# Optimization experiments

Hardware: AMD Instinct MI355X
Metric: run time of the kernel (lower is better)

The kernel has to match this reference:

```python
import jax, jax.numpy as jnp
import numpy as np

N0, N1, N2 = 200000, 100000, 50000
E0, E1 = 1600000, 800000
D_IN, H, C, K = 256, 256, 7, 40  # in_feats, n_hidden, center_num, n_classes


def setup_inputs() -> dict:
    key = jax.random.key(0)
    ks = jax.random.split(key, 11)
    s = 0.05
    inputs = jax.random.normal(ks[0], (N0, D_IN), jnp.float32)
    edge_src0 = jax.random.randint(ks[1], (E0,), 0, N0, jnp.int32)
    edge_dst0 = jax.random.randint(ks[2], (E0,), 0, N1, jnp.int32)
    edge_src1 = jax.random.randint(ks[3], (E1,), 0, N1, jnp.int32)
    edge_dst1 = jax.random.randint(ks[4], (E1,), 0, N2, jnp.int32)
    W_self0 = jax.random.normal(ks[5], (H, D_IN), jnp.float32) * s
    W_neigh0 = jax.random.normal(ks[6], (H, D_IN), jnp.float32) * s
    b0 = jnp.zeros((H,), jnp.float32)
    W_self1 = jax.random.normal(ks[7], (H, H), jnp.float32) * s
    W_neigh1 = jax.random.normal(ks[8], (H, H), jnp.float32) * s
    b1 = jnp.zeros((H,), jnp.float32)
    W_prompt = jax.random.normal(ks[9], (C, 2 * H), jnp.float32) * s
    W_pp = jax.random.normal(ks[10], (C, K, 2 * H), jnp.float32) * s
    return dict(inputs=inputs, W_self0=W_self0, W_neigh0=W_neigh0, b0=b0,
                W_self1=W_self1, W_neigh1=W_neigh1, b1=b1,
                W_prompt=W_prompt, W_pp=W_pp,
                edge_src0=edge_src0, edge_dst0=edge_dst0,
                edge_src1=edge_src1, edge_dst1=edge_dst1)


def _sage_conv(h_src, h_dst, esrc, edst, n_dst, W_self, W_neigh, b):
    # DGL SAGEConv('mean'): fc_self(h_dst) + fc_neigh(mean_{u in N(v)} h_src[u]) + bias
    msg = h_src[esrc]                                            # [E, d]
    summ = jax.ops.segment_sum(msg, edst, num_segments=n_dst)    # [n_dst, d]
    deg = jax.ops.segment_sum(jnp.ones((esrc.shape[0],), msg.dtype), edst,
                              num_segments=n_dst)                # [n_dst]
    mean = summ / jnp.maximum(deg, 1.0)[:, None]
    return h_dst @ W_self.T + mean @ W_neigh.T + b


def _forward(inputs, W_self0, W_neigh0, b0, W_self1, W_neigh1, b1,
             W_prompt, W_pp, edge_src0, edge_dst0, edge_src1, edge_dst1):
    h = inputs  # dropout=0.0 (eval): identity
    # layer 0: N0 src -> N1 dst
    h_dst = h[:N1]
    h = _sage_conv(h, h_dst, edge_src0, edge_dst0, N1, W_self0, W_neigh0, b0)
    h = jax.nn.relu(h)
    # layer 1: N1 src -> N2 dst
    h_dst = h[:N2]
    h = _sage_conv(h, h_dst, edge_src1, edge_dst1, N2, W_self1, W_neigh1, b1)
    h = jax.nn.relu(h)
    neighbor = jax.nn.relu(h_dst)
    hcat = jnp.concatenate([h, neighbor], axis=1)                # [N2, 2H]
    scores = hcat @ W_prompt.T                                   # [N2, C]
    index = jnp.argmax(scores, axis=1)                           # [N2]
    # per-cluster expert Linear, top-1 dispatch/combine
    all_out = jnp.einsum('nd,ckd->nck', hcat, W_pp)              # [N2, C, K]
    out = jnp.take_along_axis(all_out, index[:, None, None], axis=1)[:, 0, :]
    return out


def reference(inputs, W_self0, W_neigh0, b0, W_self1, W_neigh1, b1,
              W_prompt, W_pp, edge_src0, edge_dst0, edge_src1, edge_dst1):
    return _forward(inputs, W_self0, W_neigh0, b0, W_self1, W_neigh1, b1,
                    W_prompt, W_pp, edge_src0, edge_dst0, edge_src1, edge_dst1)
```

## Files before the change

kernel.cpp:

```cpp
#include <hip/hip_runtime.h>
#include <stdint.h>

typedef unsigned short u16;
typedef unsigned int   u32;
typedef float f32x4  __attribute__((ext_vector_type(4)));
typedef _Float16 f16x4 __attribute__((ext_vector_type(4)));
typedef _Float16 f16x8 __attribute__((ext_vector_type(8)));

#define NN0 200000
#define NN1 100000
#define NN2 50000
#define EE0 1600000
#define EE1 800000
#define DD  256
#define CC  7
#define KK  40
#define NHEAD 288

#define LVL2_U16 4096
#define IMG_U16  8192

static __device__ __forceinline__ void split2(float x, _Float16& t0, _Float16& t1) {
    t0 = (_Float16)x;
    t1 = (_Float16)(x - (float)t0);
}

static __device__ __forceinline__ f16x8 pack8(const _Float16* h) {
    f16x8 v;
#pragma unroll
    for (int i = 0; i < 8; ++i) v[i] = h[i];
    return v;
}

static __device__ __forceinline__ void async16(const void* g, void* l) {
    __builtin_amdgcn_global_load_lds(
        (const __attribute__((address_space(1))) void*)g,
        (__attribute__((address_space(3))) void*)l, 16, 0, 0);
}

static __device__ __forceinline__ void loadA_f32(const float* p, float* xa) {
#pragma unroll
    for (int j = 0; j < 16; j += 4) {
        float4 v = *reinterpret_cast<const float4*>(p + j);
        xa[j] = v.x; xa[j + 1] = v.y; xa[j + 2] = v.z; xa[j + 3] = v.w;
    }
}

static __device__ __forceinline__ void writeA_f32(const float* xa, u16* d, int q0, int q1) {
    _Float16 h0[16], h1v[16];
#pragma unroll
    for (int j = 0; j < 16; ++j) split2(xa[j], h0[j], h1v[j]);
    *reinterpret_cast<f16x8*>(d + q0 * 8)            = pack8(h0);
    *reinterpret_cast<f16x8*>(d + q1 * 8)            = pack8(h0 + 8);
    *reinterpret_cast<f16x8*>(d + LVL2_U16 + q0 * 8) = pack8(h1v);
    *reinterpret_cast<f16x8*>(d + LVL2_U16 + q1 * 8) = pack8(h1v + 8);
}

__global__ void hist_kernel(const int* __restrict__ dst, int* __restrict__ cnt, int n) {
    int i = blockIdx.x * blockDim.x + threadIdx.x;
    if (i < n) atomicAdd(&cnt[dst[i]], 1);
}

__global__ void scan_block_kernel(const int* __restrict__ in, int* __restrict__ out,
                                  int* __restrict__ partials, int n) {
    __shared__ int sd[256];
    int t = threadIdx.x;
    int base = blockIdx.x * 1024 + t * 4;
    int v0 = (base + 0 < n) ? in[base + 0] : 0;
    int v1 = (base + 1 < n) ? in[base + 1] : 0;
    int v2 = (base + 2 < n) ? in[base + 2] : 0;
    int v3 = (base + 3 < n) ? in[base + 3] : 0;
    int p0 = v0, p1 = p0 + v1, p2 = p1 + v2, p3 = p2 + v3;
    sd[t] = p3;
    __syncthreads();
    for (int off = 1; off < 256; off <<= 1) {
        int x = (t >= off) ? sd[t - off] : 0;
        __syncthreads();
        sd[t] += x;
        __syncthreads();
    }
    int excl = sd[t] - p3;
    if (base + 0 < n) out[base + 0] = excl + p0;
    if (base + 1 < n) out[base + 1] = excl + p1;
    if (base + 2 < n) out[base + 2] = excl + p2;
    if (base + 3 < n) out[base + 3] = excl + p3;
    if (t == 255) partials[blockIdx.x] = sd[255];
}

__global__ void scan_partials_kernel(int* __restrict__ partials, int nb) {
    __shared__ int sd[256];
    int t = threadIdx.x;
    int v = (t < nb) ? partials[t] : 0;
    sd[t] = v;
    __syncthreads();
    for (int off = 1; off < 256; off <<= 1) {
        int x = (t >= off) ? sd[t - off] : 0;
        __syncthreads();
        sd[t] += x;
        __syncthreads();
    }
    if (t < nb) partials[t] = sd[t];
}

__global__ void scan_add_kernel(int* __restrict__ out, const int* __restrict__ partials, int n) {
    int b = blockIdx.x;
    if (b == 0) return;
    int add = partials[b - 1];
    int base = b * 1024 + threadIdx.x * 4;
    if (base + 0 < n) out[base + 0] += add;
    if (base + 1 < n) out[base + 1] += add;
    if (base + 2 < n) out[base + 2] += add;
    if (base + 3 < n) out[base + 3] += add;
}

__global__ void fill_kernel(const int* __restrict__ esrc, const int* __restrict__ edst,
                            const int* __restrict__ rp, int* __restrict__ cur,
                            int* __restrict__ ss, int n) {
    int i = blockIdx.x * blockDim.x + threadIdx.x;
    if (i < n) {
        int d = edst[i];
        int p = rp[d] + atomicAdd(&cur[d], 1);
        ss[p] = esrc[i];
    }
}

__global__ void to_fp16(const float* __restrict__ in, _Float16* __restrict__ outp, long n) {
    long i = ((long)blockIdx.x * blockDim.x + threadIdx.x) * 8;
    if (i >= n) return;
    f32x4 a = *reinterpret_cast<const f32x4*>(in + i);
    f32x4 b = *reinterpret_cast<const f32x4*>(in + i + 4);
    f16x8 h;
    h[0] = (_Float16)a[0]; h[1] = (_Float16)a[1]; h[2] = (_Float16)a[2]; h[3] = (_Float16)a[3];
    h[4] = (_Float16)b[0]; h[5] = (_Float16)b[1]; h[6] = (_Float16)b[2]; h[7] = (_Float16)b[3];
    *reinterpret_cast<f16x8*>(outp + i) = h;
}

__global__ void gather_mean_fp16(const _Float16* __restrict__ Xh, const int* __restrict__ rp,
                                 const int* __restrict__ ss, float* __restrict__ mean, int ndst) {
    int wave = threadIdx.x >> 6, lane = threadIdx.x & 63;
    int d = blockIdx.x * 4 + wave;
    if (d >= ndst) return;
    int beg = rp[d], end = rp[d + 1];
    int lo4 = lane * 4;
    f32x4 a0 = (f32x4)(0.f), a1 = (f32x4)(0.f), a2 = (f32x4)(0.f), a3 = (f32x4)(0.f);
    int j = beg;
    for (; j + 8 <= end; j += 8) {
        int s0 = ss[j + 0], s1 = ss[j + 1], s2 = ss[j + 2], s3 = ss[j + 3];
        int s4 = ss[j + 4], s5 = ss[j + 5], s6 = ss[j + 6], s7 = ss[j + 7];
        f16x4 h0 = *reinterpret_cast<const f16x4*>(Xh + (size_t)s0 * DD + lo4);
        f16x4 h1 = *reinterpret_cast<const f16x4*>(Xh + (size_t)s1 * DD + lo4);
        f16x4 h2 = *reinterpret_cast<const f16x4*>(Xh + (size_t)s2 * DD + lo4);
        f16x4 h3 = *reinterpret_cast<const f16x4*>(Xh + (size_t)s3 * DD + lo4);
        f16x4 h4 = *reinterpret_cast<const f16x4*>(Xh + (size_t)s4 * DD + lo4);
        f16x4 h5 = *reinterpret_cast<const f16x4*>(Xh + (size_t)s5 * DD + lo4);
        f16x4 h6 = *reinterpret_cast<const f16x4*>(Xh + (size_t)s6 * DD + lo4);
        f16x4 h7 = *reinterpret_cast<const f16x4*>(Xh + (size_t)s7 * DD + lo4);
        a0 += __builtin_convertvector(h0, f32x4);
        a1 += __builtin_convertvector(h1, f32x4);
        a2 += __builtin_convertvector(h2, f32x4);
        a3 += __builtin_convertvector(h3, f32x4);
        a0 += __builtin_convertvector(h4, f32x4);
        a1 += __builtin_convertvector(h5, f32x4);
        a2 += __builtin_convertvector(h6, f32x4);
        a3 += __builtin_convertvector(h7, f32x4);
    }
    for (; j + 4 <= end; j += 4) {
        int s0 = ss[j + 0], s1 = ss[j + 1], s2 = ss[j + 2], s3 = ss[j + 3];
        f16x4 h0 = *reinterpret_cast<const f16x4*>(Xh + (size_t)s0 * DD + lo4);
        f16x4 h1 = *reinterpret_cast<const f16x4*>(Xh + (size_t)s1 * DD + lo4);
        f16x4 h2 = *reinterpret_cast<const f16x4*>(Xh + (size_t)s2 * DD + lo4);
        f16x4 h3 = *reinterpret_cast<const f16x4*>(Xh + (size_t)s3 * DD + lo4);
        a0 += __builtin_convertvector(h0, f32x4);
        a1 += __builtin_convertvector(h1, f32x4);
        a2 += __builtin_convertvector(h2, f32x4);
        a3 += __builtin_convertvector(h3, f32x4);
    }
    for (; j < end; ++j) {
        int s = ss[j];
        f16x4 h0 = *reinterpret_cast<const f16x4*>(Xh + (size_t)s * DD + lo4);
        a0 += __builtin_convertvector(h0, f32x4);
    }
    f32x4 s = (a0 + a1) + (a2 + a3);
    int dg = end - beg;
    float inv = 1.0f / (float)(dg > 0 ? dg : 1);
    s *= inv;
    *reinterpret_cast<f32x4*>(mean + (size_t)d * DD + lo4) = s;
}

__global__ void build_wimg(const float* __restrict__ Wa0, const float* __restrict__ Wb0,
                           const float* __restrict__ Wa1, const float* __restrict__ Wb1,
                           u16* __restrict__ img) {
    int blk = blockIdx.x;
    int layer = blk >> 5;
    int ntile = (blk >> 4) & 1;
    int chunk = blk & 15;
    const float* Wa = layer ? Wa1 : Wa0;
    const float* Wb = layer ? Wb1 : Wb0;
    int t = threadIdx.x;
    int row = t >> 1, half = t & 1;
    int n = ntile * 128 + row;
    int kg = chunk * 32 + half * 16;
    const float* W = (kg < 256) ? Wa : Wb;
    int kk = kg & 255;
    float x[16];
    loadA_f32(W + (size_t)n * 256 + kk, x);
    int rs = (row >> 1) & 3;
    int q0 = (half * 2 + 0) ^ rs;
    int q1 = (half * 2 + 1) ^ rs;
    writeA_f32(x, img + (size_t)blk * IMG_U16 + row * 32, q0, q1);
}

__global__ void build_wimg_head(const float* __restrict__ Wp, const float* __restrict__ Wpp,
                                u16* __restrict__ img) {
    int blk = blockIdx.x;
    int ntile = blk >> 4;
    int chunk = blk & 15;
    int t = threadIdx.x;
    int row = t >> 1, half = t & 1;
    int r = ntile * 128 + row;
    int kg = chunk * 32 + half * 16;
    float x[16];
    const float* src = nullptr;
    if (r < CC)                src = Wp  + (size_t)r * 512 + kg;
    else if (r < CC + CC * KK) src = Wpp + (size_t)(r - CC) * 512 + kg;
    if (src) loadA_f32(src, x);
    else {
#pragma unroll
        for (int j = 0; j < 16; ++j) x[j] = 0.f;
    }
    int rs = (row >> 1) & 3;
    int q0 = (half * 2 + 0) ^ rs;
    int q1 = (half * 2 + 1) ^ rs;
    writeA_f32(x, img + (size_t)blk * IMG_U16 + row * 32, q0, q1);
}

__global__ __launch_bounds__(256, 3) void gemm_f16(const float* __restrict__ X0,
                                                   const float* __restrict__ X1,
                                                   const u16* __restrict__ imgL,
                                                   const float* __restrict__ bias,
                                                   float* __restrict__ out,
                                                   _Float16* __restrict__ outh,
                                                   int M, int ldo, int dorelu) {
    __shared__ __align__(16) u16 Asl[2 * LVL2_U16];
    __shared__ __align__(16) u16 Bsl[2][2 * LVL2_U16];
    int t = threadIdx.x;
    int wave = t >> 6, lane = t & 63;
    int m0 = blockIdx.x * 128;
    int ntile = blockIdx.y;
    int wy = wave >> 1, wx = wave & 1;

    f32x4 acc[4][4];
#pragma unroll
    for (int i = 0; i < 4; ++i)
#pragma unroll
        for (int j = 0; j < 4; ++j) acc[i][j] = (f32x4)(0.f);

    int arow_l = t >> 1;
    int akh = t & 1;
    int arow = m0 + arow_l; if (arow >= M) arow = M - 1;
    int rsw = (arow_l >> 1) & 3;
    int q0w = (akh * 2 + 0) ^ rsw;
    int q1w = (akh * 2 + 1) ^ rsw;

    int fr = lane & 15;
    int q  = lane >> 4;
    int frm = wy * 64 + fr;
    int frn = wx * 64 + fr;

    const u16* imgT = imgL + (size_t)ntile * 16 * IMG_U16;

    float xa[16];

    auto issueB = [&](int cc, int buf) {
        const char* srcB = (const char*)(imgT + (size_t)cc * IMG_U16);
        char* dstB = (char*)Bsl[buf];
#pragma unroll
        for (int i = 0; i < 4; ++i) {
            int seg = wave * 4 + i;
            async16(srcB + seg * 1024 + lane * 16, dstB + seg * 1024 + lane * 16);
        }
    };
    auto loadA = [&](int cc) {
        const float* Xs = (cc < 8) ? X0 : X1;
        loadA_f32(Xs + (size_t)arow * 256 + (cc & 7) * 32 + akh * 16, xa);
    };
    auto writeA = [&]() {
        writeA_f32(xa, Asl + arow_l * 32, q0w, q1w);
    };

    issueB(0, 0);
    loadA(0);
    writeA();
    __syncthreads();

    for (int c = 0; c < 16; ++c) {
        int nc = c + 1;
        if (nc < 16) {
            issueB(nc, nc & 1);
            loadA(nc);
        }
        const u16* B = Bsl[c & 1];
        f16x8 bf[4][2];
#pragma unroll
        for (int ns = 0; ns < 4; ++ns) {
            int r = frn + ns * 16;
            int off = r * 32 + ((q ^ ((r >> 1) & 3))) * 8;
            bf[ns][0] = *reinterpret_cast<const f16x8*>(B + off);
            bf[ns][1] = *reinterpret_cast<const f16x8*>(B + LVL2_U16 + off);
        }
#pragma unroll
        for (int ms = 0; ms < 4; ++ms) {
            int r = frm + ms * 16;
            int off = r * 32 + ((q ^ ((r >> 1) & 3))) * 8;
            f16x8 af0 = *reinterpret_cast<const f16x8*>(Asl + off);
            f16x8 af1 = *reinterpret_cast<const f16x8*>(Asl + LVL2_U16 + off);
#pragma unroll
            for (int ns = 0; ns < 4; ++ns) {
                f32x4 a = acc[ms][ns];
                a = __builtin_amdgcn_mfma_f32_16x16x32_f16(af0, bf[ns][0], a, 0, 0, 0);
                a = __builtin_amdgcn_mfma_f32_16x16x32_f16(af0, bf[ns][1], a, 0, 0, 0);
                a = __builtin_amdgcn_mfma_f32_16x16x32_f16(af1, bf[ns][0], a, 0, 0, 0);
                acc[ms][ns] = a;
            }
        }
        __syncthreads();
        if (nc < 16) {
            writeA();
            __syncthreads();
        }
    }
#pragma unroll
    for (int ms = 0; ms < 4; ++ms) {
        int rbase = m0 + wy * 64 + ms * 16 + (lane >> 4) * 4;
#pragma unroll
        for (int ns = 0; ns < 4; ++ns) {
            int col = ntile * 128 + wx * 64 + ns * 16 + (lane & 15);
            if (col >= ldo) continue;
            float bcol = bias ? bias[col] : 0.f;
#pragma unroll
            for (int r = 0; r < 4; ++r) {
                int row = rbase + r;
                if (row < M) {
                    float v = acc[ms][ns][r] + bcol;
                    if (dorelu) v = fmaxf(v, 0.f);
                    out[(size_t)row * ldo + col] = v;
                    if (outh) outh[(size_t)row * DD + col] = (_Float16)v;
                }
            }
        }
    }
}

__global__ void select_kernel(const float* __restrict__ all, float* __restrict__ out) {
    int wave = threadIdx.x >> 6, lane = threadIdx.x & 63;
    int n = blockIdx.x * 4 + wave;
    if (n >= NN2) return;
    const float* row = all + (size_t)n * NHEAD;
    float best = row[0]; int bc = 0;
#pragma unroll
    for (int c = 1; c < CC; ++c) {
        float s = row[c];
        if (s > best) { best = s; bc = c; }
    }
    if (lane < KK) out[(size_t)n * KK + lane] = row[CC + bc * KK + lane];
}

extern "C" void kernel_launch(void* const* d_in, const int* in_sizes, int n_in,
                              void* d_out, int out_size, void* d_ws, size_t ws_size,
                              hipStream_t stream) {
    const float* inputs  = (const float*)d_in[0];
    const float* Wself0  = (const float*)d_in[1];
    const float* Wneigh0 = (const float*)d_in[2];
    const float* b0      = (const float*)d_in[3];
    const float* Wself1  = (const float*)d_in[4];
    const float* Wneigh1 = (const float*)d_in[5];
    const float* b1      = (const float*)d_in[6];
    const float* Wp      = (const float*)d_in[7];
    const float* Wpp     = (const float*)d_in[8];
    const int* es0 = (const int*)d_in[9];
    const int* ed0 = (const int*)d_in[10];
    const int* es1 = (const int*)d_in[11];
    const int* ed1 = (const int*)d_in[12];

    char* ws = (char*)d_ws;
    size_t off = 0;
    auto alloc = [&](size_t bytes) -> void* {
        void* p = (void*)(ws + off);
        off += (bytes + 255) & ~(size_t)255;
        return p;
    };
    int* cnt0 = (int*)alloc((size_t)NN1 * 4);
    int* cnt1 = (int*)alloc((size_t)NN2 * 4);
    int* cur0 = (int*)alloc((size_t)NN1 * 4);
    int* cur1 = (int*)alloc((size_t)NN2 * 4);
    int* rp0  = (int*)alloc((size_t)(NN1 + 1) * 4);
    int* rp1  = (int*)alloc((size_t)(NN2 + 1) * 4);
    int* part0 = (int*)alloc(1024);
    int* part1 = (int*)alloc(1024);
    size_t zero_bytes = off;
    int*   ss0   = (int*)alloc((size_t)EE0 * 4);
    int*   ss1   = (int*)alloc((size_t)EE1 * 4);
    u16*   wimg  = (u16*)alloc((size_t)(64 + 48) * IMG_U16 * 2);
    u16*   wimgH = wimg + (size_t)64 * IMG_U16;
    _Float16* xh = (_Float16*)alloc((size_t)NN0 * DD * 2);
    float*    h1 = (float*)xh;
    _Float16* h1h  = (_Float16*)alloc((size_t)NN1 * DD * 2);
    float* mean0 = (float*)alloc((size_t)NN1 * DD * 4);
    float* mean1 = mean0;
    float* h2    = mean0 + (size_t)NN2 * DD;
    float* allout = (float*)alloc((size_t)NN2 * NHEAD * 4);

    hipMemsetAsync(d_ws, 0, zero_bytes, stream);

    hist_kernel<<<(EE0 + 255) / 256, 256, 0, stream>>>(ed0, cnt0, EE0);
    hist_kernel<<<(EE1 + 255) / 256, 256, 0, stream>>>(ed1, cnt1, EE1);
    int nb0 = (NN1 + 1023) / 1024, nb1 = (NN2 + 1023) / 1024;
    scan_block_kernel<<<nb0, 256, 0, stream>>>(cnt0, rp0 + 1, part0, NN1);
    scan_partials_kernel<<<1, 256, 0, stream>>>(part0, nb0);
    scan_add_kernel<<<nb0, 256, 0, stream>>>(rp0 + 1, part0, NN1);
    scan_block_kernel<<<nb1, 256, 0, stream>>>(cnt1, rp1 + 1, part1, NN2);
    scan_partials_kernel<<<1, 256, 0, stream>>>(part1, nb1);
    scan_add_kernel<<<nb1, 256, 0, stream>>>(rp1 + 1, part1, NN2);
    fill_kernel<<<(EE0 + 255) / 256, 256, 0, stream>>>(es0, ed0, rp0, cur0, ss0, EE0);
    fill_kernel<<<(EE1 + 255) / 256, 256, 0, stream>>>(es1, ed1, rp1, cur1, ss1, EE1);

    build_wimg<<<64, 256, 0, stream>>>(Wself0, Wneigh0, Wself1, Wneigh1, wimg);
    build_wimg_head<<<48, 256, 0, stream>>>(Wp, Wpp, wimgH);

    long nx = (long)NN0 * DD;
    to_fp16<<<(int)(nx / 8 / 256), 256, 0, stream>>>(inputs, xh, nx);

    gather_mean_fp16<<<(NN1 + 3) / 4, 256, 0, stream>>>(xh, rp0, ss0, mean0, NN1);
    dim3 g0((NN1 + 127) / 128, 2);
    gemm_f16<<<g0, 256, 0, stream>>>(inputs, mean0, wimg, b0, h1, h1h, NN1, DD, 1);

    gather_mean_fp16<<<(NN2 + 3) / 4, 256, 0, stream>>>(h1h, rp1, ss1, mean1, NN2);
    dim3 g1((NN2 + 127) / 128, 2);
    gemm_f16<<<g1, 256, 0, stream>>>(h1, mean1, wimg + (size_t)32 * IMG_U16, b1, h2, nullptr, NN2, DD, 1);

    dim3 gh((NN2 + 127) / 128, 3);
    gemm_f16<<<gh, 256, 0, stream>>>(h2, h1, wimgH, nullptr, allout, nullptr, NN2, NHEAD, 0);
    select_kernel<<<(NN2 + 3) / 4, 256, 0, stream>>>(allout, (float*)d_out);
}
```

Measured before the change: 1.084 ms.

## Pre-split activations into swizzled fp16 hi/lo tile images for async GEMM A loads

Producers (fp16 conversion, gather-mean, and GEMM epilogues) now write activations directly as pre-swizzled hi/lo fp16 tile images, so the GEMM can load A via async global-to-LDS copies like B instead of loading fp32 and splitting in registers. The GEMM loop drops double-buffering in favour of a single buffer with a sync per chunk and raises the occupancy hint to 4 blocks. This removes per-block fp32 loads and split work from the GEMM but doubles activation storage writes and loses load/compute overlap within a block.

```diff
diff --git a/kernel.cpp b/kernel.cpp
--- a/kernel.cpp
+++ b/kernel.cpp
@@ -19,6 +19,7 @@
 
 #define LVL2_U16 4096
 #define IMG_U16  8192
+#define AIMG_STRIDE (8 * IMG_U16)
 
 static __device__ __forceinline__ void split2(float x, _Float16& t0, _Float16& t1) {
     t0 = (_Float16)x;
@@ -124,19 +125,31 @@
     }
 }
 
-__global__ void to_fp16(const float* __restrict__ in, _Float16* __restrict__ outp, long n) {
+__global__ void to_fp16_split(const float* __restrict__ in, _Float16* __restrict__ xh,
+                              u16* __restrict__ imgX, long n) {
     long i = ((long)blockIdx.x * blockDim.x + threadIdx.x) * 8;
     if (i >= n) return;
     f32x4 a = *reinterpret_cast<const f32x4*>(in + i);
     f32x4 b = *reinterpret_cast<const f32x4*>(in + i + 4);
-    f16x8 h;
-    h[0] = (_Float16)a[0]; h[1] = (_Float16)a[1]; h[2] = (_Float16)a[2]; h[3] = (_Float16)a[3];
-    h[4] = (_Float16)b[0]; h[5] = (_Float16)b[1]; h[6] = (_Float16)b[2]; h[7] = (_Float16)b[3];
-    *reinterpret_cast<f16x8*>(outp + i) = h;
+    float x[8] = {a[0], a[1], a[2], a[3], b[0], b[1], b[2], b[3]};
+    _Float16 t0[8], t1[8];
+#pragma unroll
+    for (int j = 0; j < 8; ++j) split2(x[j], t0[j], t1[j]);
+    *reinterpret_cast<f16x8*>(xh + i) = pack8(t0);
+    int row = (int)(i >> 8);
+    if (row < NN1) {
+        int k = (int)(i & 255);
+        int lrow = row & 127, ch = k >> 5;
+        int qs = ((k & 31) >> 3) ^ ((lrow >> 1) & 3);
+        u16* p = imgX + (size_t)(row >> 7) * AIMG_STRIDE + (size_t)ch * IMG_U16
+               + lrow * 32 + qs * 8;
+        *reinterpret_cast<f16x8*>(p)            = pack8(t0);
+        *reinterpret_cast<f16x8*>(p + LVL2_U16) = pack8(t1);
+    }
 }
 
 __global__ void gather_mean_fp16(const _Float16* __restrict__ Xh, const int* __restrict__ rp,
-                                 const int* __restrict__ ss, float* __restrict__ mean, int ndst) {
+                                 const int* __restrict__ ss, u16* __restrict__ imgM, int ndst) {
     int wave = threadIdx.x >> 6, lane = threadIdx.x & 63;
     int d = blockIdx.x * 4 + wave;
     if (d >= ndst) return;
@@ -184,7 +197,15 @@
     int dg = end - beg;
     float inv = 1.0f / (float)(dg > 0 ? dg : 1);
     s *= inv;
-    *reinterpret_cast<f32x4*>(mean + (size_t)d * DD + lo4) = s;
+    f16x4 t0v, t1v;
+#pragma unroll
+    for (int jj = 0; jj < 4; ++jj) { _Float16 ta, tb; split2(s[jj], ta, tb); t0v[jj] = ta; t1v[jj] = tb; }
+    int lrow = d & 127, ch = lane >> 3;
+    int qs = ((lane >> 1) & 3) ^ ((lrow >> 1) & 3);
+    u16* p = imgM + (size_t)(d >> 7) * AIMG_STRIDE + (size_t)ch * IMG_U16
+           + lrow * 32 + qs * 8 + (lane & 1) * 4;
+    *reinterpret_cast<f16x4*>(p)            = t0v;
+    *reinterpret_cast<f16x4*>(p + LVL2_U16) = t1v;
 }
 
 __global__ void build_wimg(const float* __restrict__ Wa0, const float* __restrict__ Wb0,
@@ -234,15 +255,16 @@
     writeA_f32(x, img + (size_t)blk * IMG_U16 + row * 32, q0, q1);
 }
 
-__global__ __launch_bounds__(256, 3) void gemm_f16(const float* __restrict__ X0,
-                                                   const float* __restrict__ X1,
-                                                   const u16* __restrict__ imgL,
+__global__ __launch_bounds__(256, 4) void gemm_img(const u16* __restrict__ imgA0,
+                                                   const u16* __restrict__ imgA1,
+                                                   const u16* __restrict__ imgB,
                                                    const float* __restrict__ bias,
                                                    float* __restrict__ out,
+                                                   u16* __restrict__ imgOut,
                                                    _Float16* __restrict__ outh,
                                                    int M, int ldo, int dorelu) {
-    __shared__ __align__(16) u16 Asl[2 * LVL2_U16];
-    __shared__ __align__(16) u16 Bsl[2][2 * LVL2_U16];
+    __shared__ __align__(16) u16 Asl[IMG_U16];
+    __shared__ __align__(16) u16 Bsl[IMG_U16];
     int t = threadIdx.x;
     int wave = t >> 6, lane = t & 63;
     int m0 = blockIdx.x * 128;
@@ -255,58 +277,32 @@
 #pragma unroll
         for (int j = 0; j < 4; ++j) acc[i][j] = (f32x4)(0.f);
 
-    int arow_l = t >> 1;
-    int akh = t & 1;
-    int arow = m0 + arow_l; if (arow >= M) arow = M - 1;
-    int rsw = (arow_l >> 1) & 3;
-    int q0w = (akh * 2 + 0) ^ rsw;
-    int q1w = (akh * 2 + 1) ^ rsw;
-
     int fr = lane & 15;
     int q  = lane >> 4;
     int frm = wy * 64 + fr;
     int frn = wx * 64 + fr;
 
-    const u16* imgT = imgL + (size_t)ntile * 16 * IMG_U16;
-
-    float xa[16];
-
-    auto issueB = [&](int cc, int buf) {
-        const char* srcB = (const char*)(imgT + (size_t)cc * IMG_U16);
-        char* dstB = (char*)Bsl[buf];
+    const u16* imgBT = imgB + (size_t)ntile * 16 * IMG_U16;
+    size_t mboff = (size_t)blockIdx.x * AIMG_STRIDE;
+
+    for (int c = 0; c < 16; ++c) {
+        const char* sB = (const char*)(imgBT + (size_t)c * IMG_U16);
+        const char* sA = (const char*)((c < 8) ? imgA0 + mboff + (size_t)c * IMG_U16
+                                               : imgA1 + mboff + (size_t)(c - 8) * IMG_U16);
 #pragma unroll
         for (int i = 0; i < 4; ++i) {
-            int seg = wave * 4 + i;
-            async16(srcB + seg * 1024 + lane * 16, dstB + seg * 1024 + lane * 16);
+            int off = (wave * 4 + i) * 1024 + lane * 16;
+            async16(sB + off, (char*)Bsl + off);
+            async16(sA + off, (char*)Asl + off);
         }
-    };
-    auto loadA = [&](int cc) {
-        const float* Xs = (cc < 8) ? X0 : X1;
-        loadA_f32(Xs + (size_t)arow * 256 + (cc & 7) * 32 + akh * 16, xa);
-    };
-    auto writeA = [&]() {
-        writeA_f32(xa, Asl + arow_l * 32, q0w, q1w);
-    };
-
-    issueB(0, 0);
-    loadA(0);
-    writeA();
-    __syncthreads();
-
-    for (int c = 0; c < 16; ++c) {
-        int nc = c + 1;
-        if (nc < 16) {
-            issueB(nc, nc & 1);
-            loadA(nc);
-        }
-        const u16* B = Bsl[c & 1];
+        __syncthreads();
         f16x8 bf[4][2];
 #pragma unroll
         for (int ns = 0; ns < 4; ++ns) {
             int r = frn + ns * 16;
             int off = r * 32 + ((q ^ ((r >> 1) & 3))) * 8;
-            bf[ns][0] = *reinterpret_cast<const f16x8*>(B + off);
-            bf[ns][1] = *reinterpret_cast<const f16x8*>(B + LVL2_U16 + off);
+            bf[ns][0] = *reinterpret_cast<const f16x8*>(Bsl + off);
+            bf[ns][1] = *reinterpret_cast<const f16x8*>(Bsl + LVL2_U16 + off);
         }
 #pragma unroll
         for (int ms = 0; ms < 4; ++ms) {
@@ -324,10 +320,6 @@
             }
         }
         __syncthreads();
-        if (nc < 16) {
-            writeA();
-            __syncthreads();
-        }
     }
 #pragma unroll
     for (int ms = 0; ms < 4; ++ms) {
@@ -335,16 +327,24 @@
 #pragma unroll
         for (int ns = 0; ns < 4; ++ns) {
             int col = ntile * 128 + wx * 64 + ns * 16 + (lane & 15);
-            if (col >= ldo) continue;
             float bcol = bias ? bias[col] : 0.f;
 #pragma unroll
             for (int r = 0; r < 4; ++r) {
                 int row = rbase + r;
-                if (row < M) {
-                    float v = acc[ms][ns][r] + bcol;
-                    if (dorelu) v = fmaxf(v, 0.f);
-                    out[(size_t)row * ldo + col] = v;
-                    if (outh) outh[(size_t)row * DD + col] = (_Float16)v;
+                if (row >= M) continue;
+                float v = acc[ms][ns][r] + bcol;
+                if (dorelu) v = fmaxf(v, 0.f);
+                if (out && col < ldo) out[(size_t)row * ldo + col] = v;
+                if (outh) outh[(size_t)row * DD + col] = (_Float16)v;
+                if (imgOut) {
+                    _Float16 t0, t1;
+                    split2(v, t0, t1);
+                    int lrow = row & 127, ch = col >> 5, kk = col & 31;
+                    int qs = (kk >> 3) ^ ((lrow >> 1) & 3);
+                    u16* p = imgOut + (size_t)(row >> 7) * AIMG_STRIDE + (size_t)ch * IMG_U16
+                           + lrow * 32 + qs * 8 + (kk & 7);
+                    p[0]        = __builtin_bit_cast(u16, t0);
+                    p[LVL2_U16] = __builtin_bit_cast(u16, t1);
                 }
             }
         }
@@ -402,13 +402,15 @@
     int*   ss1   = (int*)alloc((size_t)EE1 * 4);
     u16*   wimg  = (u16*)alloc((size_t)(64 + 48) * IMG_U16 * 2);
     u16*   wimgH = wimg + (size_t)64 * IMG_U16;
-    _Float16* xh = (_Float16*)alloc((size_t)NN0 * DD * 2);
-    float*    h1 = (float*)xh;
-    _Float16* h1h  = (_Float16*)alloc((size_t)NN1 * DD * 2);
-    float* mean0 = (float*)alloc((size_t)NN1 * DD * 4);
-    float* mean1 = mean0;
-    float* h2    = mean0 + (size_t)NN2 * DD;
-    float* allout = (float*)alloc((size_t)NN2 * NHEAD * 4);
+    const int MB1 = (NN1 + 127) / 128;
+    const int MB2 = (NN2 + 127) / 128;
+    u16* imgX0   = (u16*)alloc((size_t)MB1 * AIMG_STRIDE * 2);
+    u16* imgMean = (u16*)alloc((size_t)MB1 * AIMG_STRIDE * 2);
+    u16* imgH1   = (u16*)alloc((size_t)MB1 * AIMG_STRIDE * 2);
+    _Float16* h1h = (_Float16*)alloc((size_t)NN1 * DD * 2);
+    u16* imgH2   = (u16*)alloc((size_t)MB2 * AIMG_STRIDE * 2);
+    _Float16* xh = (_Float16*)imgH1;
+    float* allout = (float*)imgX0;
 
     hipMemsetAsync(d_ws, 0, zero_bytes, stream);
 
@@ -428,17 +430,20 @@
     build_wimg_head<<<48, 256, 0, stream>>>(Wp, Wpp, wimgH);
 
     long nx = (long)NN0 * DD;
-    to_fp16<<<(int)(nx / 8 / 256), 256, 0, stream>>>(inputs, xh, nx);
-
-    gather_mean_fp16<<<(NN1 + 3) / 4, 256, 0, stream>>>(xh, rp0, ss0, mean0, NN1);
-    dim3 g0((NN1 + 127) / 128, 2);
-    gemm_f16<<<g0, 256, 0, stream>>>(inputs, mean0, wimg, b0, h1, h1h, NN1, DD, 1);
-
-    gather_mean_fp16<<<(NN2 + 3) / 4, 256, 0, stream>>>(h1h, rp1, ss1, mean1, NN2);
-    dim3 g1((NN2 + 127) / 128, 2);
-    gemm_f16<<<g1, 256, 0, stream>>>(h1, mean1, wimg + (size_t)32 * IMG_U16, b1, h2, nullptr, NN2, DD, 1);
-
-    dim3 gh((NN2 + 127) / 128, 3);
-    gemm_f16<<<gh, 256, 0, stream>>>(h2, h1, wimgH, nullptr, allout, nullptr, NN2, NHEAD, 0);
+    to_fp16_split<<<(int)(nx / 8 / 256), 256, 0, stream>>>(inputs, xh, imgX0, nx);
+
+    gather_mean_fp16<<<(NN1 + 3) / 4, 256, 0, stream>>>(xh, rp0, ss0, imgMean, NN1);
+    dim3 g0(MB1, 2);
+    gemm_img<<<g0, 256, 0, stream>>>(imgX0, imgMean, wimg, b0,
+                                     nullptr, imgH1, h1h, NN1, DD, 1);
+
+    gather_mean_fp16<<<(NN2 + 3) / 4, 256, 0, stream>>>(h1h, rp1, ss1, imgMean, NN2);
+    dim3 g1(MB2, 2);
+    gemm_img<<<g1, 256, 0, stream>>>(imgH1, imgMean, wimg + (size_t)32 * IMG_U16, b1,
+                                     nullptr, imgH2, nullptr, NN2, DD, 1);
+
+    dim3 gh(MB2, 3);
+    gemm_img<<<gh, 256, 0, stream>>>(imgH2, imgH1, wimgH, nullptr,
+                                     allout, nullptr, nullptr, NN2, NHEAD, 0);
     select_kernel<<<(NN2 + 3) / 4, 256, 0, stream>>>(allout, (float*)d_out);
 }
```

New measurement: 1.065 ms. Within noise of the previous version (-1.8%).
